# Kernel optimization log

Hardware: AMD Instinct MI355X
Metric: run time of the kernel (lower is better)

The kernel has to match this reference:

```python
import jax, jax.numpy as jnp
import numpy as np

DIM = 128
H = 8
HD = DIM // H
NL = 6
DFF = 2048
EPS = 1e-5
S2S_STEPS = 6


def _ln(x, g, b):
    m = jnp.mean(x, -1, keepdims=True)
    v = jnp.mean(jnp.square(x - m), -1, keepdims=True)
    return (x - m) / jnp.sqrt(v + EPS) * g + b


def _lstm_step(x, h, c, wih, whh, bih, bhh):
    # torch LSTM gate order: i, f, g, o
    gates = x @ wih.T + bih + h @ whh.T + bhh
    i, f, g, o = jnp.split(gates, 4, axis=-1)
    c = jax.nn.sigmoid(f) * c + jax.nn.sigmoid(i) * jnp.tanh(g)
    h = jax.nn.sigmoid(o) * jnp.tanh(c)
    return h, c


def setup_inputs() -> dict:
    key = jax.random.key(0)
    ks = iter(jax.random.split(key, 16))
    n = lambda shape: jax.random.normal(next(ks), shape, jnp.float32) * 0.02
    inp = {
        "data": jax.random.normal(next(ks), (64, 256, 3), jnp.float32),
        "lin0_w": n((DIM, 3)), "lin0_b": jnp.zeros((DIM,), jnp.float32),
        "attn_in_w": n((NL, 3 * DIM, DIM)), "attn_in_b": jnp.zeros((NL, 3 * DIM), jnp.float32),
        "attn_out_w": n((NL, DIM, DIM)), "attn_out_b": jnp.zeros((NL, DIM), jnp.float32),
        "ln1_g": jnp.ones((NL, DIM), jnp.float32), "ln1_b": jnp.zeros((NL, DIM), jnp.float32),
        "ff_w1": n((NL, DFF, DIM)), "ff_b1": jnp.zeros((NL, DFF), jnp.float32),
        "ff_w2": n((NL, DIM, DFF)), "ff_b2": jnp.zeros((NL, DIM), jnp.float32),
        "ln2_g": jnp.ones((NL, DIM), jnp.float32), "ln2_b": jnp.zeros((NL, DIM), jnp.float32),
        "s2s_wih": n((4 * DIM, 2 * DIM)), "s2s_whh": n((4 * DIM, DIM)),
        "s2s_bih": jnp.zeros((4 * DIM,), jnp.float32), "s2s_bhh": jnp.zeros((4 * DIM,), jnp.float32),
        "mem_wih": n((4 * DIM, 2 * DIM)), "mem_whh": n((4 * DIM, DIM)),
        "mem_bih": jnp.zeros((4 * DIM,), jnp.float32), "mem_bhh": jnp.zeros((4 * DIM,), jnp.float32),
        "lin1_w": n((DIM, DIM)), "lin1_b": jnp.zeros((DIM,), jnp.float32),
        "lin3_w": n((1, DIM)), "lin3_b": jnp.zeros((1,), jnp.float32),
    }
    return inp


def reference(data, lin0_w, lin0_b, attn_in_w, attn_in_b, attn_out_w, attn_out_b,
              ln1_g, ln1_b, ff_w1, ff_b1, ff_w2, ff_b2, ln2_g, ln2_b,
              s2s_wih, s2s_whh, s2s_bih, s2s_bhh,
              mem_wih, mem_whh, mem_bih, mem_bhh,
              lin1_w, lin1_b, lin3_w, lin3_b):
    x = jax.nn.relu(data @ lin0_w.T + lin0_b)  # [S=64, B=256, D]
    S, B, _ = x.shape
    # torch TransformerEncoder with batch_first=False: attention over axis 0,
    # axis 1 is the transformer batch. Post-norm layers (norm_first=False), relu FFN.
    for l in range(NL):
        qkv = x @ attn_in_w[l].T + attn_in_b[l]
        q, k, v = jnp.split(qkv, 3, axis=-1)
        q = q.reshape(S, B, H, HD)
        k = k.reshape(S, B, H, HD)
        v = v.reshape(S, B, H, HD)
        scores = jnp.einsum('sbhd,tbhd->bhst', q, k) / np.float32(np.sqrt(HD))
        attn = jax.nn.softmax(scores, axis=-1)
        ao = jnp.einsum('bhst,tbhd->sbhd', attn, v).reshape(S, B, DIM)
        x = _ln(x + ao @ attn_out_w[l].T + attn_out_b[l], ln1_g[l], ln1_b[l])
        ff = jax.nn.relu(x @ ff_w1[l].T + ff_b1[l]) @ ff_w2[l].T + ff_b2[l]
        x = _ln(x + ff, ln2_g[l], ln2_b[l])
    # Set2Set pooling: bidxs assign segment = axis-0 index for each block of
    # num_atoms consecutive rows of flatten(out,0,1), i.e. pool over axis 1.
    q_star = jnp.zeros((S, 2 * DIM), x.dtype)
    h = jnp.zeros((S, DIM), x.dtype)
    c = jnp.zeros((S, DIM), x.dtype)
    for _ in range(S2S_STEPS):
        h, c = _lstm_step(q_star, h, c, s2s_wih, s2s_whh, s2s_bih, s2s_bhh)
        e = jnp.einsum('bnd,bd->bn', x, h)          # [S, num_atoms]
        a = jax.nn.softmax(e, axis=-1)              # segment softmax (uniform segs)
        r = jnp.einsum('bn,bnd->bd', a, x)          # segment weighted sum
        q_star = jnp.concatenate([h, r], axis=-1)   # [S, 2D]
    # memory LSTM: seq_len 1, zero initial state (states=None branch)
    hx = jnp.zeros((S, DIM), x.dtype)
    cx = jnp.zeros((S, DIM), x.dtype)
    hx, cx = _lstm_step(q_star, hx, cx, mem_wih, mem_whh, mem_bih, mem_bhh)
    o = jax.nn.relu(hx @ lin1_w.T + lin1_b)
    v_out = (o @ lin3_w.T + lin3_b)[None]  # [1, S, 1]
    return v_out, hx[None], cx[None]
```

## Files before the change

### kernel.cpp

```cpp
#include <hip/hip_runtime.h>
#include <math.h>


typedef _Float16 __attribute__((ext_vector_type(8))) f16x8;
typedef __attribute__((ext_vector_type(4))) float f32x4;
typedef _Float16 __attribute__((ext_vector_type(2))) h16x2;

__device__ __forceinline__ unsigned short f2h(float f) {
  union { _Float16 h; unsigned short s; } x; x.h = (_Float16)f; return x.s;
}
__device__ __forceinline__ float h2f(unsigned short u) {
  union { unsigned short s; _Float16 h; } x; x.s = u; return (float)x.h;
}
__device__ __forceinline__ unsigned packh(float a, float b) {
  return (unsigned)f2h(a) | ((unsigned)f2h(b) << 16);
}
__device__ __forceinline__ float hlo(unsigned u) {
  union { unsigned short s; _Float16 h; } x; x.s = (unsigned short)(u & 0xffff);
  return (float)x.h;
}
__device__ __forceinline__ float hhi(unsigned u) {
  union { unsigned short s; _Float16 h; } x; x.s = (unsigned short)(u >> 16);
  return (float)x.h;
}
__device__ __forceinline__ float fdot2u(unsigned a, unsigned b, float c) {
#if __has_builtin(__builtin_amdgcn_fdot2)
  union U { unsigned u; h16x2 h; };
  U x, y; x.u = a; y.u = b;
  return __builtin_amdgcn_fdot2(x.h, y.h, c, false);
#else
  return c + hlo(a) * hlo(b) + hhi(a) * hhi(b);
#endif
}
__device__ __forceinline__ float sigf(float x) { return 1.f / (1.f + expf(-x)); }

__device__ __forceinline__ void gl2lds16(const void* g, void* l) {
  __builtin_amdgcn_global_load_lds(
      (const __attribute__((address_space(1))) unsigned int*)g,
      (__attribute__((address_space(3))) unsigned int*)l, 16, 0, 0);
}

__global__ __launch_bounds__(256) void convw_kernel(
    const float* __restrict__ aiw, const float* __restrict__ aow,
    const float* __restrict__ w1, const float* __restrict__ w2,
    const float* __restrict__ wih, const float* __restrict__ whh,
    const float* __restrict__ mwih,
    unsigned short* __restrict__ o0, unsigned short* __restrict__ o1,
    unsigned short* __restrict__ o2, unsigned short* __restrict__ o3,
    unsigned short* __restrict__ o4, unsigned short* __restrict__ o5,
    unsigned short* __restrict__ o6) {
  int i = blockIdx.x * 256 + threadIdx.x;
  if (i < 294912) {
    int l = i / 49152, o = i % 49152;
    int j = o & 7, fr = (o >> 3) & 15, fq = (o >> 7) & 3, ks = (o >> 9) & 3,
        rb = o >> 11;
    o0[i] = f2h(aiw[l * 49152 + (rb * 16 + fr) * 128 + ks * 32 + fq * 8 + j]);
  } else if (i < 393216) {
    int ii = i - 294912;
    int l = ii / 16384, o = ii % 16384;
    int j = o & 7, fr = (o >> 3) & 15, fq = (o >> 7) & 3, ks = (o >> 9) & 3,
        rb = o >> 11;
    o1[ii] = f2h(aow[l * 16384 + (rb * 16 + fr) * 128 + ks * 32 + fq * 8 + j]);
  } else if (i < 1966080) {
    int ii = i - 393216;
    int l = ii >> 18, o = ii & 262143;
    int j = o & 7, fr = (o >> 3) & 15, fq = (o >> 7) & 3, ks = (o >> 9) & 3,
        rb = o >> 11;
    o2[ii] = f2h(w1[l * 262144 + (rb * 16 + fr) * 128 + ks * 32 + fq * 8 + j]);
  } else if (i < 3538944) {
    int ii = i - 1966080;
    int l = ii >> 18, o = ii & 262143;
    int j = o & 7, fr = (o >> 3) & 15, fq = (o >> 7) & 3, ks = (o >> 9) & 63,
        rb = o >> 15;
    o3[ii] = f2h(w2[l * 262144 + (rb * 16 + fr) * 2048 + ks * 32 + fq * 8 + j]);
  } else if (i < 3670016) {
    int j = i - 3538944; o4[j] = f2h(wih[j]);
  } else if (i < 3735552) {
    int j = i - 3670016; o5[j] = f2h(whh[j]);
  } else {
    int j = i - 3735552; o6[j] = f2h(mwih[j]);
  }
}

__global__ __launch_bounds__(256) void lin0_kernel(
    const float* __restrict__ data, const float* __restrict__ w,
    const float* __restrict__ b, float* __restrict__ x,
    unsigned short* __restrict__ xb) {
  int i = blockIdx.x * 256 + threadIdx.x;
  int n = i >> 7, d = i & 127;
  float v = b[d] + data[n * 3 + 0] * w[d * 3 + 0]
                 + data[n * 3 + 1] * w[d * 3 + 1]
                 + data[n * 3 + 2] * w[d * 3 + 2];
  v = fmaxf(v, 0.0f);
  x[i] = v;
  xb[i] = f2h(v);
}

__global__ __launch_bounds__(256, 2) void layer_kernel(
    const unsigned short* __restrict__ xbg,
    const unsigned short* __restrict__ wqkv, const float* __restrict__ bqkv,
    const unsigned short* __restrict__ wout, const float* __restrict__ bout,
    const float* __restrict__ ln1g, const float* __restrict__ ln1b,
    const unsigned short* __restrict__ w1, const float* __restrict__ b1,
    const unsigned short* __restrict__ w2, const float* __restrict__ b2,
    const float* __restrict__ ln2g, const float* __restrict__ ln2b,
    float* __restrict__ xio, unsigned short* __restrict__ xbo) {
  __shared__ __align__(16) unsigned short Xs[64 * 128];
  __shared__ __align__(16) unsigned short QKP[16384];
  __shared__ __align__(16) unsigned short VT[128 * 64];
  __shared__ __align__(16) uint4 zchunk;
  __shared__ float psum[4][32], psq[4][32];
  __shared__ float2 stats[32];

  unsigned short* Qs = QKP;
  unsigned short* Ks2 = QKP + 8192;

  int tid = threadIdx.x, w = tid >> 6, lane = tid & 63;
  int b = blockIdx.x >> 1, half = blockIdx.x & 1;
  int r4 = lane >> 4, cs = lane & 15;
  int fr = lane & 15, fq = lane >> 4;

  if (tid == 0) zchunk = make_uint4(0u, 0u, 0u, 0u);

#pragma unroll
  for (int i = 0; i < 4; i++) {
    int issue = w * 4 + i;
    int row = issue * 4 + r4;
    int g = cs ^ (row & 7);
    gl2lds16(xbg + (size_t)(row * 256 + b) * 128 + g * 8,
             (char*)Xs + issue * 1024);
  }
  __syncthreads();

  f16x8 xfragA[4][4];
#pragma unroll
  for (int ks = 0; ks < 4; ks++)
#pragma unroll
    for (int mi = 0; mi < 4; mi++) {
      int row = mi * 16 + fr;
      int kq = (ks * 4 + fq) ^ (row & 7);
      xfragA[ks][mi] = *(const f16x8*)(Xs + row * 128 + kq * 8);
    }

  {
    f32x4 acc[4][4];
#pragma unroll
    for (int i = 0; i < 4; i++)
#pragma unroll
      for (int j = 0; j < 4; j++) acc[i][j] = (f32x4){0.f, 0.f, 0.f, 0.f};
#pragma unroll
    for (int ks = 0; ks < 4; ks++) {
      f16x8 bf[4];
#pragma unroll
      for (int ni = 0; ni < 4; ni++)
        bf[ni] = *(const f16x8*)(wqkv + (w * 4 + ni) * 2048 + ks * 512 +
                                 fq * 128 + fr * 8);
#pragma unroll
      for (int mi = 0; mi < 4; mi++)
#pragma unroll
        for (int ni = 0; ni < 4; ni++)
          acc[mi][ni] = __builtin_amdgcn_mfma_f32_16x16x32_f16(
              xfragA[ks][mi], bf[ni], acc[mi][ni], 0, 0, 0);
    }
#pragma unroll
    for (int ni = 0; ni < 4; ni++) {
      int c = (w * 4 + ni) * 16 + fr;
      float bv = bqkv[c];
      unsigned short* dst = (c < 128) ? Qs : Ks2;
      int cc = c & 127;
#pragma unroll
      for (int mi = 0; mi < 4; mi++)
#pragma unroll
        for (int r = 0; r < 4; r++) {
          int row = mi * 16 + fq * 4 + r;
          dst[row * 128 + (((cc >> 3) ^ (row & 7)) << 3) + (cc & 7)] =
              f2h(acc[mi][ni][r] + bv);
        }
    }
  }
  __syncthreads();

  {
    f32x4 acc[2][4];
#pragma unroll
    for (int i = 0; i < 2; i++)
#pragma unroll
      for (int j = 0; j < 4; j++) acc[i][j] = (f32x4){0.f, 0.f, 0.f, 0.f};
#pragma unroll
    for (int ks = 0; ks < 4; ks++) {
      f16x8 bf[2];
#pragma unroll
      for (int fi = 0; fi < 2; fi++)
        bf[fi] = *(const f16x8*)(wqkv + (16 + w * 2 + fi) * 2048 + ks * 512 +
                                 fq * 128 + fr * 8);
#pragma unroll
      for (int fi = 0; fi < 2; fi++)
#pragma unroll
        for (int mi = 0; mi < 4; mi++)
          acc[fi][mi] = __builtin_amdgcn_mfma_f32_16x16x32_f16(
              xfragA[ks][mi], bf[fi], acc[fi][mi], 0, 0, 0);
    }
#pragma unroll
    for (int fi = 0; fi < 2; fi++) {
      int f = (w * 2 + fi) * 16 + fr;
      float bv = bqkv[256 + f];
#pragma unroll
      for (int mi = 0; mi < 4; mi++)
#pragma unroll
        for (int r = 0; r < 4; r++) {
          int srow = mi * 16 + fq * 4 + r;
          VT[f * 64 + (((srow >> 3) ^ (f & 7)) << 3) + (srow & 7)] =
              f2h(acc[fi][mi][r] + bv);
        }
    }
  }
  __syncthreads();

  {
    f16x8 afH[2][2], bfH[2][4];
#pragma unroll
    for (int hi = 0; hi < 2; hi++) {
      int h = w * 2 + hi;
#pragma unroll
      for (int mi2 = 0; mi2 < 2; mi2++) {
        int rowg = half * 32 + mi2 * 16 + fr;
        const unsigned short* pa =
            (fq < 2) ? (Qs + rowg * 128 + (((h * 2 + fq) ^ (rowg & 7)) << 3))
                     : (const unsigned short*)&zchunk;
        afH[hi][mi2] = *(const f16x8*)pa;
      }
#pragma unroll
      for (int ti = 0; ti < 4; ti++) {
        int trow = ti * 16 + fr;
        const unsigned short* pb =
            (fq < 2) ? (Ks2 + trow * 128 + (((h * 2 + fq) ^ (trow & 7)) << 3))
                     : (const unsigned short*)&zchunk;
        bfH[hi][ti] = *(const f16x8*)pb;
      }
    }
    __syncthreads();

#pragma unroll
    for (int hi = 0; hi < 2; hi++) {
      int h = w * 2 + hi;
      unsigned short* Pb = QKP + (w * 2 + hi) * 2048;
      f32x4 sc[2][4];
#pragma unroll
      for (int i = 0; i < 2; i++)
#pragma unroll
        for (int j = 0; j < 4; j++) sc[i][j] = (f32x4){0.f, 0.f, 0.f, 0.f};
#pragma unroll
      for (int mi2 = 0; mi2 < 2; mi2++)
#pragma unroll
        for (int ti = 0; ti < 4; ti++)
          sc[mi2][ti] = __builtin_amdgcn_mfma_f32_16x16x32_f16(
              afH[hi][mi2], bfH[hi][ti], sc[mi2][ti], 0, 0, 0);
#pragma unroll
      for (int mi2 = 0; mi2 < 2; mi2++) {
#pragma unroll
        for (int r = 0; r < 4; r++) {
          float m = -1e30f;
#pragma unroll
          for (int ti = 0; ti < 4; ti++) m = fmaxf(m, sc[mi2][ti][r]);
          m = fmaxf(m, __shfl_xor(m, 1, 64));
          m = fmaxf(m, __shfl_xor(m, 2, 64));
          m = fmaxf(m, __shfl_xor(m, 4, 64));
          m = fmaxf(m, __shfl_xor(m, 8, 64));
          m *= 0.25f;
          float ss = 0.f;
#pragma unroll
          for (int ti = 0; ti < 4; ti++) {
            float p = expf(sc[mi2][ti][r] * 0.25f - m);
            sc[mi2][ti][r] = p;
            ss += p;
          }
          ss += __shfl_xor(ss, 1, 64);
          ss += __shfl_xor(ss, 2, 64);
          ss += __shfl_xor(ss, 4, 64);
          ss += __shfl_xor(ss, 8, 64);
          float inv = 1.f / ss;
          int prow = mi2 * 16 + fq * 4 + r;
#pragma unroll
          for (int ti = 0; ti < 4; ti++) {
            int t = ti * 16 + fr;
            Pb[prow * 64 + (((t >> 3) ^ (prow & 7)) << 3) + (t & 7)] =
                f2h(sc[mi2][ti][r] * inv);
          }
        }
      }
      f32x4 po[2];
#pragma unroll
      for (int i = 0; i < 2; i++) po[i] = (f32x4){0.f, 0.f, 0.f, 0.f};
#pragma unroll
      for (int ks2 = 0; ks2 < 2; ks2++) {
        f16x8 af[2], bf;
#pragma unroll
        for (int si2 = 0; si2 < 2; si2++) {
          int prow = si2 * 16 + fr;
          int kq = (ks2 * 4 + fq) ^ (prow & 7);
          af[si2] = *(const f16x8*)(Pb + prow * 64 + kq * 8);
        }
        {
          int vrow = h * 16 + fr;
          int kq = (ks2 * 4 + fq) ^ (vrow & 7);
          bf = *(const f16x8*)(VT + vrow * 64 + kq * 8);
        }
#pragma unroll
        for (int si2 = 0; si2 < 2; si2++)
          po[si2] = __builtin_amdgcn_mfma_f32_16x16x32_f16(af[si2], bf,
                                                           po[si2], 0, 0, 0);
      }
#pragma unroll
      for (int si2 = 0; si2 < 2; si2++)
#pragma unroll
        for (int r = 0; r < 4; r++) {
          int arow = si2 * 16 + fq * 4 + r;
          int c = h * 16 + fr;
          Xs[arow * 128 + (((c >> 3) ^ (arow & 7)) << 3) + (c & 7)] =
              f2h(po[si2][r]);
        }
    }
  }
  __syncthreads();

  float vv4[2][2][4];
  {
    f32x4 acc[2][2];
#pragma unroll
    for (int i = 0; i < 2; i++)
#pragma unroll
      for (int j = 0; j < 2; j++) acc[i][j] = (f32x4){0.f, 0.f, 0.f, 0.f};
#pragma unroll
    for (int ks = 0; ks < 4; ks++) {
      f16x8 af[2], bwo[2];
#pragma unroll
      for (int si2 = 0; si2 < 2; si2++) {
        int rowl = si2 * 16 + fr;
        int kq = (ks * 4 + fq) ^ (rowl & 7);
        af[si2] = *(const f16x8*)(Xs + rowl * 128 + kq * 8);
      }
#pragma unroll
      for (int ni = 0; ni < 2; ni++)
        bwo[ni] = *(const f16x8*)(wout + (w * 2 + ni) * 2048 + ks * 512 +
                                  fq * 128 + fr * 8);
#pragma unroll
      for (int si2 = 0; si2 < 2; si2++)
#pragma unroll
        for (int ni = 0; ni < 2; ni++)
          acc[si2][ni] = __builtin_amdgcn_mfma_f32_16x16x32_f16(
              af[si2], bwo[ni], acc[si2][ni], 0, 0, 0);
    }
    float sums[2][4], sqs[2][4];
#pragma unroll
    for (int si2 = 0; si2 < 2; si2++)
#pragma unroll
      for (int r = 0; r < 4; r++) { sums[si2][r] = 0.f; sqs[si2][r] = 0.f; }
#pragma unroll
    for (int ni = 0; ni < 2; ni++) {
      int c = (w * 2 + ni) * 16 + fr;
      float bv = bout[c];
#pragma unroll
      for (int si2 = 0; si2 < 2; si2++)
#pragma unroll
        for (int r = 0; r < 4; r++) {
          int rowl = si2 * 16 + fq * 4 + r;
          int rowg = half * 32 + rowl;
          float v = acc[si2][ni][r] + bv + xio[(size_t)(rowg * 256 + b) * 128 + c];
          vv4[ni][si2][r] = v;
          sums[si2][r] += v;
          sqs[si2][r] += v * v;
        }
    }
#pragma unroll
    for (int d = 1; d < 16; d <<= 1) {
#pragma unroll
      for (int si2 = 0; si2 < 2; si2++)
#pragma unroll
        for (int r = 0; r < 4; r++) {
          sums[si2][r] += __shfl_xor(sums[si2][r], d, 64);
          sqs[si2][r] += __shfl_xor(sqs[si2][r], d, 64);
        }
    }
    if (fr == 0) {
#pragma unroll
      for (int si2 = 0; si2 < 2; si2++)
#pragma unroll
        for (int r = 0; r < 4; r++) {
          int rowl = si2 * 16 + fq * 4 + r;
          psum[w][rowl] = sums[si2][r];
          psq[w][rowl] = sqs[si2][r];
        }
    }
    __syncthreads();
    if (tid < 32) {
      float S = 0.f, Q = 0.f;
#pragma unroll
      for (int ww = 0; ww < 4; ww++) { S += psum[ww][tid]; Q += psq[ww][tid]; }
      float m = S * (1.f / 128.f);
      float var = Q * (1.f / 128.f) - m * m;
      stats[tid] = make_float2(m, rsqrtf(var + 1e-5f));
    }
    __syncthreads();
#pragma unroll
    for (int ni = 0; ni < 2; ni++) {
      int c = (w * 2 + ni) * 16 + fr;
      float gl = ln1g[c], bl = ln1b[c];
#pragma unroll
      for (int si2 = 0; si2 < 2; si2++)
#pragma unroll
        for (int r = 0; r < 4; r++) {
          int rowl = si2 * 16 + fq * 4 + r;
          float2 st2 = stats[rowl];
          float y = (vv4[ni][si2][r] - st2.x) * st2.y * gl + bl;
          Xs[rowl * 128 + (((c >> 3) ^ (rowl & 7)) << 3) + (c & 7)] = f2h(y);
        }
    }
  }
  __syncthreads();

  f16x8 xfragF[4][2];
#pragma unroll
  for (int ks = 0; ks < 4; ks++)
#pragma unroll
    for (int mi2 = 0; mi2 < 2; mi2++) {
      int rowl = mi2 * 16 + fr;
      int kq = (ks * 4 + fq) ^ (rowl & 7);
      xfragF[ks][mi2] = *(const f16x8*)(Xs + rowl * 128 + kq * 8);
    }

  f32x4 acc2[2][2];
#pragma unroll
  for (int i = 0; i < 2; i++)
#pragma unroll
    for (int j = 0; j < 2; j++) acc2[i][j] = (f32x4){0.f, 0.f, 0.f, 0.f};

  for (int c = 0; c < 16; c++) {
    unsigned short* Hcur = QKP + (c & 1) * 4096;
    f32x4 acc1[2][2];
#pragma unroll
    for (int i = 0; i < 2; i++)
#pragma unroll
      for (int j = 0; j < 2; j++) acc1[i][j] = (f32x4){0.f, 0.f, 0.f, 0.f};
#pragma unroll
    for (int ks = 0; ks < 4; ks++) {
      f16x8 b1f[2];
#pragma unroll
      for (int ni = 0; ni < 2; ni++)
        b1f[ni] = *(const f16x8*)(w1 + (size_t)(c * 8 + w * 2 + ni) * 2048 +
                                  ks * 512 + fq * 128 + fr * 8);
#pragma unroll
      for (int mi2 = 0; mi2 < 2; mi2++)
#pragma unroll
        for (int ni = 0; ni < 2; ni++)
          acc1[mi2][ni] = __builtin_amdgcn_mfma_f32_16x16x32_f16(
              xfragF[ks][mi2], b1f[ni], acc1[mi2][ni], 0, 0, 0);
    }
#pragma unroll
    for (int ni = 0; ni < 2; ni++) {
      int col = (w * 2 + ni) * 16 + fr;
      float bv = b1[c * 128 + col];
#pragma unroll
      for (int mi2 = 0; mi2 < 2; mi2++)
#pragma unroll
        for (int r = 0; r < 4; r++) {
          int rowl = mi2 * 16 + fq * 4 + r;
          Hcur[rowl * 128 + (((col >> 3) ^ (rowl & 7)) << 3) + (col & 7)] =
              f2h(fmaxf(acc1[mi2][ni][r] + bv, 0.f));
        }
    }
    __syncthreads();
#pragma unroll
    for (int ks = 0; ks < 4; ks++) {
      f16x8 af[2], b2f[2];
#pragma unroll
      for (int si2 = 0; si2 < 2; si2++) {
        int rowl = si2 * 16 + fr;
        int kq = (ks * 4 + fq) ^ (rowl & 7);
        af[si2] = *(const f16x8*)(Hcur + rowl * 128 + kq * 8);
      }
#pragma unroll
      for (int ni = 0; ni < 2; ni++)
        b2f[ni] = *(const f16x8*)(w2 + (size_t)(w * 2 + ni) * 32768 +
                                  (c * 4 + ks) * 512 + fq * 128 + fr * 8);
#pragma unroll
      for (int si2 = 0; si2 < 2; si2++)
#pragma unroll
        for (int ni = 0; ni < 2; ni++)
          acc2[si2][ni] = __builtin_amdgcn_mfma_f32_16x16x32_f16(
              af[si2], b2f[ni], acc2[si2][ni], 0, 0, 0);
    }
  }

  {
    float vvo[2][2][4];
    float sums[2][4], sqs[2][4];
#pragma unroll
    for (int si2 = 0; si2 < 2; si2++)
#pragma unroll
      for (int r = 0; r < 4; r++) { sums[si2][r] = 0.f; sqs[si2][r] = 0.f; }
#pragma unroll
    for (int ni = 0; ni < 2; ni++) {
      int c = (w * 2 + ni) * 16 + fr;
      float bv = b2[c];
#pragma unroll
      for (int si2 = 0; si2 < 2; si2++)
#pragma unroll
        for (int r = 0; r < 4; r++) {
          int rowl = si2 * 16 + fq * 4 + r;
          float resid =
              h2f(Xs[rowl * 128 + (((c >> 3) ^ (rowl & 7)) << 3) + (c & 7)]);
          float v = acc2[si2][ni][r] + bv + resid;
          vvo[ni][si2][r] = v;
          sums[si2][r] += v;
          sqs[si2][r] += v * v;
        }
    }
#pragma unroll
    for (int d = 1; d < 16; d <<= 1) {
#pragma unroll
      for (int si2 = 0; si2 < 2; si2++)
#pragma unroll
        for (int r = 0; r < 4; r++) {
          sums[si2][r] += __shfl_xor(sums[si2][r], d, 64);
          sqs[si2][r] += __shfl_xor(sqs[si2][r], d, 64);
        }
    }
    if (fr == 0) {
#pragma unroll
      for (int si2 = 0; si2 < 2; si2++)
#pragma unroll
        for (int r = 0; r < 4; r++) {
          int rowl = si2 * 16 + fq * 4 + r;
          psum[w][rowl] = sums[si2][r];
          psq[w][rowl] = sqs[si2][r];
        }
    }
    __syncthreads();
    if (tid < 32) {
      float S = 0.f, Q = 0.f;
#pragma unroll
      for (int ww = 0; ww < 4; ww++) { S += psum[ww][tid]; Q += psq[ww][tid]; }
      float m = S * (1.f / 128.f);
      float var = Q * (1.f / 128.f) - m * m;
      stats[tid] = make_float2(m, rsqrtf(var + 1e-5f));
    }
    __syncthreads();
#pragma unroll
    for (int ni = 0; ni < 2; ni++) {
      int c = (w * 2 + ni) * 16 + fr;
      float gl = ln2g[c], bl = ln2b[c];
#pragma unroll
      for (int si2 = 0; si2 < 2; si2++)
#pragma unroll
        for (int r = 0; r < 4; r++) {
          int rowl = si2 * 16 + fq * 4 + r;
          float2 st = stats[rowl];
          float y = (vvo[ni][si2][r] - st.x) * st.y * gl + bl;
          size_t o = (size_t)((half * 32 + rowl) * 256 + b) * 128 + c;
          xio[o] = y;
          xbo[o] = f2h(y);
        }
    }
  }
}

__global__ __launch_bounds__(512, 1) void s2s_kernel(
    const unsigned short* __restrict__ xb,
    const unsigned short* __restrict__ wihh,
    const unsigned short* __restrict__ whhh,
    const float* __restrict__ bih, const float* __restrict__ bhh,
    const unsigned short* __restrict__ mwihh,
    const float* __restrict__ mbih, const float* __restrict__ mbhh,
    const float* __restrict__ l1w, const float* __restrict__ l1b,
    const float* __restrict__ l3w, const float* __restrict__ l3b,
    float* __restrict__ out) {
  __shared__ __align__(16) unsigned xl[256 * 65];
  __shared__ __align__(16) unsigned qu[128];
  __shared__ __align__(16) float cst[128];
  __shared__ __align__(16) float gates[512];
  __shared__ __align__(16) float red[256];
  __shared__ __align__(16) float aw[256];
  int s = blockIdx.x, t = threadIdx.x, lane = t & 63, w = t >> 6;

  uint4 wreg[32], ureg[16];
  {
    const uint4* wp = (const uint4*)(wihh + (size_t)t * 256);
#pragma unroll
    for (int i = 0; i < 32; i++) wreg[i] = wp[i];
    const uint4* up = (const uint4*)(whhh + (size_t)t * 128);
#pragma unroll
    for (int i = 0; i < 16; i++) ureg[i] = up[i];
  }

  const uint4* xs4 = (const uint4*)(xb + (size_t)s * 32768);
#pragma unroll
  for (int it = 0; it < 8; it++) {
    int f = it * 512 + t;
    uint4 v = xs4[f];
    int n = f >> 4, jc = (f & 15) * 4;
    unsigned* dst = xl + n * 65 + jc;
    dst[0] = v.x; dst[1] = v.y; dst[2] = v.z; dst[3] = v.w;
  }
  if (t < 128) cst[t] = 0.f;
  __syncthreads();

  const uint4* q4 = (const uint4*)qu;
  float bsum = bih[t] + bhh[t];

  for (int step = 0; step < 6; step++) {
    if (step > 0) {
      float a0 = 0.f, a1 = 0.f, a2 = 0.f, a3 = 0.f;
#pragma unroll
      for (int i = 0; i < 16; i++) {
        uint4 qv = q4[i];
        a0 = fdot2u(wreg[i].x, qv.x, a0);
        a1 = fdot2u(wreg[i].y, qv.y, a1);
        a2 = fdot2u(wreg[i].z, qv.z, a2);
        a3 = fdot2u(wreg[i].w, qv.w, a3);
        a0 = fdot2u(ureg[i].x, qv.x, a0);
        a1 = fdot2u(ureg[i].y, qv.y, a1);
        a2 = fdot2u(ureg[i].z, qv.z, a2);
        a3 = fdot2u(ureg[i].w, qv.w, a3);
      }
#pragma unroll
      for (int i = 16; i < 32; i++) {
        uint4 qv = q4[i];
        a0 = fdot2u(wreg[i].x, qv.x, a0);
        a1 = fdot2u(wreg[i].y, qv.y, a1);
        a2 = fdot2u(wreg[i].z, qv.z, a2);
        a3 = fdot2u(wreg[i].w, qv.w, a3);
      }
      gates[t] = bsum + ((a0 + a1) + (a2 + a3));
    } else {
      gates[t] = bsum;
    }
    __syncthreads();
    if (t < 128) {
      float ig = sigf(gates[t]), fg = sigf(gates[128 + t]);
      float gg = tanhf(gates[256 + t]), og = sigf(gates[384 + t]);
      float cn = fg * cst[t] + ig * gg;
      cst[t] = cn;
      float hn = og * tanhf(cn);
      float hp = __shfl_xor(hn, 1, 64);
      if ((t & 1) == 0) qu[t >> 1] = packh(hn, hp);
    }
    __syncthreads();
    if (step > 0) {
      int n = t >> 1, p = t & 1;
      const unsigned* xr = xl + n * 65 + p * 32;
      float e0 = 0.f, e1 = 0.f;
#pragma unroll 8
      for (int i = 0; i < 32; i += 2) {
        e0 = fdot2u(xr[i], qu[p * 32 + i], e0);
        e1 = fdot2u(xr[i + 1], qu[p * 32 + i + 1], e1);
      }
      float e = e0 + e1;
      e += __shfl_xor(e, 1, 64);
      if (p == 0) red[n] = e;
      __syncthreads();
      float v0 = red[lane], v1 = red[64 + lane];
      float v2 = red[128 + lane], v3 = red[192 + lane];
      float m = fmaxf(fmaxf(v0, v1), fmaxf(v2, v3));
#pragma unroll
      for (int d = 1; d < 64; d <<= 1) m = fmaxf(m, __shfl_xor(m, d, 64));
      float p0 = expf(v0 - m), p1 = expf(v1 - m);
      float p2 = expf(v2 - m), p3 = expf(v3 - m);
      float ss = p0 + p1 + p2 + p3;
#pragma unroll
      for (int d = 1; d < 64; d <<= 1) ss += __shfl_xor(ss, d, 64);
      float Sinv = 1.f / ss;
      if (w == 0) {
        aw[lane] = p0 * Sinv; aw[64 + lane] = p1 * Sinv;
        aw[128 + lane] = p2 * Sinv; aw[192 + lane] = p3 * Sinv;
      }
    } else {
      if (t < 256) aw[t] = 1.f / 256.f;
    }
    __syncthreads();
    {
      int d = t & 127, grp = t >> 7;
      const unsigned* xc = xl + grp * 64 * 65 + (d >> 1);
      int hi = d & 1;
      const float* ap = aw + grp * 64;
      float r = 0.f;
#pragma unroll 8
      for (int n2 = 0; n2 < 64; n2++) {
        unsigned u = xc[n2 * 65];
        r += ap[n2] * (hi ? hhi(u) : hlo(u));
      }
      gates[t] = r;
    }
    __syncthreads();
    if (t < 128) {
      float rd = gates[t] + gates[128 + t] + gates[256 + t] + gates[384 + t];
      float rp = __shfl_xor(rd, 1, 64);
      if ((t & 1) == 0) qu[64 + (t >> 1)] = packh(rd, rp);
    }
    __syncthreads();
  }
  {
    float a0 = 0.f, a1 = 0.f, a2 = 0.f, a3 = 0.f;
    const uint4* mp = (const uint4*)(mwihh + (size_t)t * 256);
#pragma unroll 8
    for (int i = 0; i < 32; i++) {
      uint4 wv = mp[i], qv = q4[i];
      a0 = fdot2u(wv.x, qv.x, a0);
      a1 = fdot2u(wv.y, qv.y, a1);
      a2 = fdot2u(wv.z, qv.z, a2);
      a3 = fdot2u(wv.w, qv.w, a3);
    }
    gates[t] = mbih[t] + mbhh[t] + ((a0 + a1) + (a2 + a3));
  }
  __syncthreads();
  if (t < 128) {
    float ig = sigf(gates[t]);
    float gg = tanhf(gates[256 + t]);
    float og = sigf(gates[384 + t]);
    float cx = ig * gg;
    float hx = og * tanhf(cx);
    cst[t] = hx;
    out[64 + s * 128 + t] = hx;
    out[64 + 8192 + s * 128 + t] = cx;
  }
  __syncthreads();
  if (t < 128) {
    float acc = l1b[t];
    const float4* w4 = (const float4*)(l1w + (size_t)t * 128);
    const float4* h4 = (const float4*)cst;
#pragma unroll 8
    for (int k = 0; k < 32; k++) {
      float4 a = w4[k], b = h4[k];
      acc += a.x * b.x + a.y * b.y + a.z * b.z + a.w * b.w;
    }
    red[t] = fmaxf(acc, 0.f) * l3w[t];
  } else if (t < 256) {
    red[t] = 0.f;
  }
  __syncthreads();
  for (int off = 128; off; off >>= 1) {
    if (t < off) red[t] += red[t + off];
    __syncthreads();
  }
  if (t == 0) out[s] = red[0] + l3b[0];
}

extern "C" void kernel_launch(void* const* d_in, const int* in_sizes, int n_in,
                              void* d_out, int out_size, void* d_ws,
                              size_t ws_size, hipStream_t stream) {
  const float* data       = (const float*)d_in[0];
  const float* lin0_w     = (const float*)d_in[1];
  const float* lin0_b     = (const float*)d_in[2];
  const float* attn_in_w  = (const float*)d_in[3];
  const float* attn_in_b  = (const float*)d_in[4];
  const float* attn_out_w = (const float*)d_in[5];
  const float* attn_out_b = (const float*)d_in[6];
  const float* ln1_g      = (const float*)d_in[7];
  const float* ln1_b      = (const float*)d_in[8];
  const float* ff_w1      = (const float*)d_in[9];
  const float* ff_b1      = (const float*)d_in[10];
  const float* ff_w2      = (const float*)d_in[11];
  const float* ff_b2      = (const float*)d_in[12];
  const float* ln2_g      = (const float*)d_in[13];
  const float* ln2_b      = (const float*)d_in[14];
  const float* s2s_wih    = (const float*)d_in[15];
  const float* s2s_whh    = (const float*)d_in[16];
  const float* s2s_bih    = (const float*)d_in[17];
  const float* s2s_bhh    = (const float*)d_in[18];
  const float* mem_wih    = (const float*)d_in[19];
  const float* mem_bih    = (const float*)d_in[21];
  const float* mem_bhh    = (const float*)d_in[22];
  const float* lin1_w     = (const float*)d_in[23];
  const float* lin1_b     = (const float*)d_in[24];
  const float* lin3_w     = (const float*)d_in[25];
  const float* lin3_b     = (const float*)d_in[26];
  float* out = (float*)d_out;

  char* p = (char*)d_ws;
  float* x = (float*)p;                      p += (size_t)16384 * 128 * 4;
  unsigned short* xb = (unsigned short*)p;   p += (size_t)16384 * 128 * 2;
  unsigned short* wqkv = (unsigned short*)p; p += (size_t)294912 * 2;
  unsigned short* wout = (unsigned short*)p; p += (size_t)98304 * 2;
  unsigned short* w1h = (unsigned short*)p;  p += (size_t)1572864 * 2;
  unsigned short* w2h = (unsigned short*)p;  p += (size_t)1572864 * 2;
  unsigned short* wihh = (unsigned short*)p; p += (size_t)131072 * 2;
  unsigned short* whhh = (unsigned short*)p; p += (size_t)65536 * 2;
  unsigned short* mwihh = (unsigned short*)p; p += (size_t)131072 * 2;

  convw_kernel<<<15104, 256, 0, stream>>>(
      attn_in_w, attn_out_w, ff_w1, ff_w2, s2s_wih, s2s_whh, mem_wih,
      wqkv, wout, w1h, w2h, wihh, whhh, mwihh);
  lin0_kernel<<<8192, 256, 0, stream>>>(data, lin0_w, lin0_b, x, xb);

  for (int l = 0; l < 6; l++) {
    layer_kernel<<<512, 256, 0, stream>>>(
        xb, wqkv + (size_t)l * 49152, attn_in_b + l * 384,
        wout + (size_t)l * 16384, attn_out_b + l * 128,
        ln1_g + l * 128, ln1_b + l * 128,
        w1h + (size_t)l * 262144, ff_b1 + l * 2048,
        w2h + (size_t)l * 262144, ff_b2 + l * 128,
        ln2_g + l * 128, ln2_b + l * 128, x, xb);
  }

  s2s_kernel<<<64, 512, 0, stream>>>(
      xb, wihh, whhh, s2s_bih, s2s_bhh,
      mwihh, mem_bih, mem_bhh, lin1_w, lin1_b, lin3_w, lin3_b, out);
}
```

Baseline: 461.5 us.

## Use 8 waves per layer block and overlay shared memory buffers

The transformer layer kernel now runs 512 threads (8 waves) per block instead of 256. Each wave handles one attention head and one 16-column slice of every projection and FFN chunk, and the QKV projection is merged into a single pass with 3 column tiles per wave. Shared memory is reorganised into one overlaid buffer, with Q stored only for this block's half of the rows, which cuts LDS use so more blocks can stay resident. The aim is higher occupancy and more latency hiding, at the cost of extra barriers, a smaller per-wave MFMA tile, and every wave recomputing all 64 rows of K and V.

```diff
diff --git a/kernel.cpp b/kernel.cpp
--- a/kernel.cpp
+++ b/kernel.cpp
@@ -96,7 +96,7 @@
   xb[i] = f2h(v);
 }
 
-__global__ __launch_bounds__(256, 2) void layer_kernel(
+__global__ __launch_bounds__(512, 4) void layer_kernel(
     const unsigned short* __restrict__ xbg,
     const unsigned short* __restrict__ wqkv, const float* __restrict__ bqkv,
     const unsigned short* __restrict__ wout, const float* __restrict__ bout,
@@ -105,26 +105,28 @@
     const unsigned short* __restrict__ w2, const float* __restrict__ b2,
     const float* __restrict__ ln2g, const float* __restrict__ ln2b,
     float* __restrict__ xio, unsigned short* __restrict__ xbo) {
-  __shared__ __align__(16) unsigned short Xs[64 * 128];
-  __shared__ __align__(16) unsigned short QKP[16384];
-  __shared__ __align__(16) unsigned short VT[128 * 64];
-  __shared__ __align__(16) uint4 zchunk;
-  __shared__ float psum[4][32], psq[4][32];
-  __shared__ float2 stats[32];
-
-  unsigned short* Qs = QKP;
-  unsigned short* Ks2 = QKP + 8192;
+  __shared__ __align__(16) unsigned short SM[25736];
+  unsigned short* Xs = SM;
+  unsigned short* Qs = SM + 4096;
+  unsigned short* Ks = SM + 8192;
+  unsigned short* VT = SM + 16384;
+  unsigned short* AOs = SM + 16384;
+  unsigned short* Xn = SM;
+  float* psum = (float*)(SM + 24576);
+  float* psq = (float*)(SM + 25088);
+  float2* stats = (float2*)(SM + 25600);
+  uint4* zch = (uint4*)(SM + 25728);
 
   int tid = threadIdx.x, w = tid >> 6, lane = tid & 63;
   int b = blockIdx.x >> 1, half = blockIdx.x & 1;
   int r4 = lane >> 4, cs = lane & 15;
   int fr = lane & 15, fq = lane >> 4;
 
-  if (tid == 0) zchunk = make_uint4(0u, 0u, 0u, 0u);
-
-#pragma unroll
-  for (int i = 0; i < 4; i++) {
-    int issue = w * 4 + i;
+  if (tid == 0) *zch = make_uint4(0u, 0u, 0u, 0u);
+
+#pragma unroll
+  for (int i = 0; i < 2; i++) {
+    int issue = w * 2 + i;
     int row = issue * 4 + r4;
     int g = cs ^ (row & 7);
     gl2lds16(xbg + (size_t)(row * 256 + b) * 128 + g * 8,
@@ -141,236 +143,206 @@
       int kq = (ks * 4 + fq) ^ (row & 7);
       xfragA[ks][mi] = *(const f16x8*)(Xs + row * 128 + kq * 8);
     }
+  __syncthreads();
 
   {
-    f32x4 acc[4][4];
+    f32x4 acc[4][3];
 #pragma unroll
     for (int i = 0; i < 4; i++)
 #pragma unroll
-      for (int j = 0; j < 4; j++) acc[i][j] = (f32x4){0.f, 0.f, 0.f, 0.f};
+      for (int j = 0; j < 3; j++) acc[i][j] = (f32x4){0.f, 0.f, 0.f, 0.f};
 #pragma unroll
     for (int ks = 0; ks < 4; ks++) {
-      f16x8 bf[4];
-#pragma unroll
-      for (int ni = 0; ni < 4; ni++)
-        bf[ni] = *(const f16x8*)(wqkv + (w * 4 + ni) * 2048 + ks * 512 +
-                                 fq * 128 + fr * 8);
+      f16x8 bf[3];
+#pragma unroll
+      for (int ni = 0; ni < 3; ni++)
+        bf[ni] = *(const f16x8*)(wqkv + (size_t)(w * 3 + ni) * 2048 +
+                                 ks * 512 + fq * 128 + fr * 8);
 #pragma unroll
       for (int mi = 0; mi < 4; mi++)
 #pragma unroll
-        for (int ni = 0; ni < 4; ni++)
+        for (int ni = 0; ni < 3; ni++)
           acc[mi][ni] = __builtin_amdgcn_mfma_f32_16x16x32_f16(
               xfragA[ks][mi], bf[ni], acc[mi][ni], 0, 0, 0);
     }
 #pragma unroll
-    for (int ni = 0; ni < 4; ni++) {
-      int c = (w * 4 + ni) * 16 + fr;
+    for (int ni = 0; ni < 3; ni++) {
+      int c = (w * 3 + ni) * 16 + fr;
       float bv = bqkv[c];
-      unsigned short* dst = (c < 128) ? Qs : Ks2;
-      int cc = c & 127;
-#pragma unroll
-      for (int mi = 0; mi < 4; mi++)
-#pragma unroll
-        for (int r = 0; r < 4; r++) {
-          int row = mi * 16 + fq * 4 + r;
-          dst[row * 128 + (((cc >> 3) ^ (row & 7)) << 3) + (cc & 7)] =
-              f2h(acc[mi][ni][r] + bv);
-        }
-    }
-  }
-  __syncthreads();
-
-  {
-    f32x4 acc[2][4];
-#pragma unroll
-    for (int i = 0; i < 2; i++)
-#pragma unroll
-      for (int j = 0; j < 4; j++) acc[i][j] = (f32x4){0.f, 0.f, 0.f, 0.f};
-#pragma unroll
-    for (int ks = 0; ks < 4; ks++) {
-      f16x8 bf[2];
-#pragma unroll
-      for (int fi = 0; fi < 2; fi++)
-        bf[fi] = *(const f16x8*)(wqkv + (16 + w * 2 + fi) * 2048 + ks * 512 +
-                                 fq * 128 + fr * 8);
-#pragma unroll
-      for (int fi = 0; fi < 2; fi++)
-#pragma unroll
-        for (int mi = 0; mi < 4; mi++)
-          acc[fi][mi] = __builtin_amdgcn_mfma_f32_16x16x32_f16(
-              xfragA[ks][mi], bf[fi], acc[fi][mi], 0, 0, 0);
-    }
-#pragma unroll
-    for (int fi = 0; fi < 2; fi++) {
-      int f = (w * 2 + fi) * 16 + fr;
-      float bv = bqkv[256 + f];
-#pragma unroll
-      for (int mi = 0; mi < 4; mi++)
-#pragma unroll
-        for (int r = 0; r < 4; r++) {
-          int srow = mi * 16 + fq * 4 + r;
-          VT[f * 64 + (((srow >> 3) ^ (f & 7)) << 3) + (srow & 7)] =
-              f2h(acc[fi][mi][r] + bv);
-        }
-    }
-  }
-  __syncthreads();
-
-  {
-    f16x8 afH[2][2], bfH[2][4];
-#pragma unroll
-    for (int hi = 0; hi < 2; hi++) {
-      int h = w * 2 + hi;
-#pragma unroll
-      for (int mi2 = 0; mi2 < 2; mi2++) {
-        int rowg = half * 32 + mi2 * 16 + fr;
-        const unsigned short* pa =
-            (fq < 2) ? (Qs + rowg * 128 + (((h * 2 + fq) ^ (rowg & 7)) << 3))
-                     : (const unsigned short*)&zchunk;
-        afH[hi][mi2] = *(const f16x8*)pa;
-      }
-#pragma unroll
-      for (int ti = 0; ti < 4; ti++) {
-        int trow = ti * 16 + fr;
-        const unsigned short* pb =
-            (fq < 2) ? (Ks2 + trow * 128 + (((h * 2 + fq) ^ (trow & 7)) << 3))
-                     : (const unsigned short*)&zchunk;
-        bfH[hi][ti] = *(const f16x8*)pb;
-      }
-    }
-    __syncthreads();
-
-#pragma unroll
-    for (int hi = 0; hi < 2; hi++) {
-      int h = w * 2 + hi;
-      unsigned short* Pb = QKP + (w * 2 + hi) * 2048;
-      f32x4 sc[2][4];
-#pragma unroll
-      for (int i = 0; i < 2; i++)
-#pragma unroll
-        for (int j = 0; j < 4; j++) sc[i][j] = (f32x4){0.f, 0.f, 0.f, 0.f};
-#pragma unroll
-      for (int mi2 = 0; mi2 < 2; mi2++)
-#pragma unroll
-        for (int ti = 0; ti < 4; ti++)
-          sc[mi2][ti] = __builtin_amdgcn_mfma_f32_16x16x32_f16(
-              afH[hi][mi2], bfH[hi][ti], sc[mi2][ti], 0, 0, 0);
-#pragma unroll
-      for (int mi2 = 0; mi2 < 2; mi2++) {
-#pragma unroll
-        for (int r = 0; r < 4; r++) {
-          float m = -1e30f;
-#pragma unroll
-          for (int ti = 0; ti < 4; ti++) m = fmaxf(m, sc[mi2][ti][r]);
-          m = fmaxf(m, __shfl_xor(m, 1, 64));
-          m = fmaxf(m, __shfl_xor(m, 2, 64));
-          m = fmaxf(m, __shfl_xor(m, 4, 64));
-          m = fmaxf(m, __shfl_xor(m, 8, 64));
-          m *= 0.25f;
-          float ss = 0.f;
-#pragma unroll
-          for (int ti = 0; ti < 4; ti++) {
-            float p = expf(sc[mi2][ti][r] * 0.25f - m);
-            sc[mi2][ti][r] = p;
-            ss += p;
-          }
-          ss += __shfl_xor(ss, 1, 64);
-          ss += __shfl_xor(ss, 2, 64);
-          ss += __shfl_xor(ss, 4, 64);
-          ss += __shfl_xor(ss, 8, 64);
-          float inv = 1.f / ss;
-          int prow = mi2 * 16 + fq * 4 + r;
-#pragma unroll
-          for (int ti = 0; ti < 4; ti++) {
-            int t = ti * 16 + fr;
-            Pb[prow * 64 + (((t >> 3) ^ (prow & 7)) << 3) + (t & 7)] =
-                f2h(sc[mi2][ti][r] * inv);
+      if (c < 128) {
+#pragma unroll
+        for (int mi2 = 0; mi2 < 2; mi2++) {
+          int mi = half * 2 + mi2;
+#pragma unroll
+          for (int r = 0; r < 4; r++) {
+            int prow = mi2 * 16 + fq * 4 + r;
+            Qs[prow * 128 + (((c >> 3) ^ (prow & 7)) << 3) + (c & 7)] =
+                f2h(acc[mi][ni][r] + bv);
           }
         }
-      }
-      f32x4 po[2];
-#pragma unroll
-      for (int i = 0; i < 2; i++) po[i] = (f32x4){0.f, 0.f, 0.f, 0.f};
-#pragma unroll
-      for (int ks2 = 0; ks2 < 2; ks2++) {
-        f16x8 af[2], bf;
-#pragma unroll
-        for (int si2 = 0; si2 < 2; si2++) {
-          int prow = si2 * 16 + fr;
-          int kq = (ks2 * 4 + fq) ^ (prow & 7);
-          af[si2] = *(const f16x8*)(Pb + prow * 64 + kq * 8);
+      } else if (c < 256) {
+        int cc = c - 128;
+#pragma unroll
+        for (int mi = 0; mi < 4; mi++)
+#pragma unroll
+          for (int r = 0; r < 4; r++) {
+            int row = mi * 16 + fq * 4 + r;
+            Ks[row * 128 + (((cc >> 3) ^ (row & 7)) << 3) + (cc & 7)] =
+                f2h(acc[mi][ni][r] + bv);
+          }
+      } else {
+        int f = c - 256;
+#pragma unroll
+        for (int mi = 0; mi < 4; mi++)
+#pragma unroll
+          for (int r = 0; r < 4; r++) {
+            int srow = mi * 16 + fq * 4 + r;
+            VT[f * 64 + (((srow >> 3) ^ (f & 7)) << 3) + (srow & 7)] =
+                f2h(acc[mi][ni][r] + bv);
+          }
+      }
+    }
+  }
+  __syncthreads();
+
+  f32x4 po[2];
+  {
+    int h = w;
+    f16x8 afH[2], bfH[4];
+#pragma unroll
+    for (int mi2 = 0; mi2 < 2; mi2++) {
+      int qrow = mi2 * 16 + fr;
+      const unsigned short* pa =
+          (fq < 2) ? (Qs + qrow * 128 + (((h * 2 + fq) ^ (qrow & 7)) << 3))
+                   : (const unsigned short*)zch;
+      afH[mi2] = *(const f16x8*)pa;
+    }
+#pragma unroll
+    for (int ti = 0; ti < 4; ti++) {
+      int trow = ti * 16 + fr;
+      const unsigned short* pb =
+          (fq < 2) ? (Ks + trow * 128 + (((h * 2 + fq) ^ (trow & 7)) << 3))
+                   : (const unsigned short*)zch;
+      bfH[ti] = *(const f16x8*)pb;
+    }
+    __syncthreads();
+
+    unsigned short* Pb = SM + w * 2048;
+    f32x4 sc[2][4];
+#pragma unroll
+    for (int i = 0; i < 2; i++)
+#pragma unroll
+      for (int j = 0; j < 4; j++) sc[i][j] = (f32x4){0.f, 0.f, 0.f, 0.f};
+#pragma unroll
+    for (int mi2 = 0; mi2 < 2; mi2++)
+#pragma unroll
+      for (int ti = 0; ti < 4; ti++)
+        sc[mi2][ti] = __builtin_amdgcn_mfma_f32_16x16x32_f16(
+            afH[mi2], bfH[ti], sc[mi2][ti], 0, 0, 0);
+#pragma unroll
+    for (int mi2 = 0; mi2 < 2; mi2++) {
+#pragma unroll
+      for (int r = 0; r < 4; r++) {
+        float m = -1e30f;
+#pragma unroll
+        for (int ti = 0; ti < 4; ti++) m = fmaxf(m, sc[mi2][ti][r]);
+        m = fmaxf(m, __shfl_xor(m, 1, 64));
+        m = fmaxf(m, __shfl_xor(m, 2, 64));
+        m = fmaxf(m, __shfl_xor(m, 4, 64));
+        m = fmaxf(m, __shfl_xor(m, 8, 64));
+        m *= 0.25f;
+        float ss = 0.f;
+#pragma unroll
+        for (int ti = 0; ti < 4; ti++) {
+          float p = expf(sc[mi2][ti][r] * 0.25f - m);
+          sc[mi2][ti][r] = p;
+          ss += p;
         }
-        {
-          int vrow = h * 16 + fr;
-          int kq = (ks2 * 4 + fq) ^ (vrow & 7);
-          bf = *(const f16x8*)(VT + vrow * 64 + kq * 8);
+        ss += __shfl_xor(ss, 1, 64);
+        ss += __shfl_xor(ss, 2, 64);
+        ss += __shfl_xor(ss, 4, 64);
+        ss += __shfl_xor(ss, 8, 64);
+        float inv = 1.f / ss;
+        int prow = mi2 * 16 + fq * 4 + r;
+#pragma unroll
+        for (int ti = 0; ti < 4; ti++) {
+          int t = ti * 16 + fr;
+          Pb[prow * 64 + (((t >> 3) ^ (prow & 7)) << 3) + (t & 7)] =
+              f2h(sc[mi2][ti][r] * inv);
         }
-#pragma unroll
-        for (int si2 = 0; si2 < 2; si2++)
-          po[si2] = __builtin_amdgcn_mfma_f32_16x16x32_f16(af[si2], bf,
-                                                           po[si2], 0, 0, 0);
+      }
+    }
+#pragma unroll
+    for (int i = 0; i < 2; i++) po[i] = (f32x4){0.f, 0.f, 0.f, 0.f};
+#pragma unroll
+    for (int ks2 = 0; ks2 < 2; ks2++) {
+      f16x8 af[2], bf;
+#pragma unroll
+      for (int si2 = 0; si2 < 2; si2++) {
+        int prow = si2 * 16 + fr;
+        int kq = (ks2 * 4 + fq) ^ (prow & 7);
+        af[si2] = *(const f16x8*)(Pb + prow * 64 + kq * 8);
+      }
+      {
+        int vrow = h * 16 + fr;
+        int kq = (ks2 * 4 + fq) ^ (vrow & 7);
+        bf = *(const f16x8*)(VT + vrow * 64 + kq * 8);
       }
 #pragma unroll
       for (int si2 = 0; si2 < 2; si2++)
-#pragma unroll
-        for (int r = 0; r < 4; r++) {
-          int arow = si2 * 16 + fq * 4 + r;
-          int c = h * 16 + fr;
-          Xs[arow * 128 + (((c >> 3) ^ (arow & 7)) << 3) + (c & 7)] =
-              f2h(po[si2][r]);
-        }
-    }
-  }
-  __syncthreads();
-
-  float vv4[2][2][4];
+        po[si2] = __builtin_amdgcn_mfma_f32_16x16x32_f16(af[si2], bf, po[si2],
+                                                         0, 0, 0);
+    }
+  }
+  __syncthreads();
   {
-    f32x4 acc[2][2];
-#pragma unroll
-    for (int i = 0; i < 2; i++)
-#pragma unroll
-      for (int j = 0; j < 2; j++) acc[i][j] = (f32x4){0.f, 0.f, 0.f, 0.f};
+    int h = w;
+#pragma unroll
+    for (int si2 = 0; si2 < 2; si2++)
+#pragma unroll
+      for (int r = 0; r < 4; r++) {
+        int arow = si2 * 16 + fq * 4 + r;
+        int c = h * 16 + fr;
+        AOs[arow * 128 + (((c >> 3) ^ (arow & 7)) << 3) + (c & 7)] =
+            f2h(po[si2][r]);
+      }
+  }
+  __syncthreads();
+
+  {
+    f32x4 acc[2];
+#pragma unroll
+    for (int i = 0; i < 2; i++) acc[i] = (f32x4){0.f, 0.f, 0.f, 0.f};
 #pragma unroll
     for (int ks = 0; ks < 4; ks++) {
-      f16x8 af[2], bwo[2];
+      f16x8 af[2];
 #pragma unroll
       for (int si2 = 0; si2 < 2; si2++) {
         int rowl = si2 * 16 + fr;
         int kq = (ks * 4 + fq) ^ (rowl & 7);
-        af[si2] = *(const f16x8*)(Xs + rowl * 128 + kq * 8);
-      }
-#pragma unroll
-      for (int ni = 0; ni < 2; ni++)
-        bwo[ni] = *(const f16x8*)(wout + (w * 2 + ni) * 2048 + ks * 512 +
+        af[si2] = *(const f16x8*)(AOs + rowl * 128 + kq * 8);
+      }
+      f16x8 bwo = *(const f16x8*)(wout + (size_t)w * 2048 + ks * 512 +
                                   fq * 128 + fr * 8);
 #pragma unroll
       for (int si2 = 0; si2 < 2; si2++)
-#pragma unroll
-        for (int ni = 0; ni < 2; ni++)
-          acc[si2][ni] = __builtin_amdgcn_mfma_f32_16x16x32_f16(
-              af[si2], bwo[ni], acc[si2][ni], 0, 0, 0);
-    }
-    float sums[2][4], sqs[2][4];
+        acc[si2] = __builtin_amdgcn_mfma_f32_16x16x32_f16(af[si2], bwo,
+                                                          acc[si2], 0, 0, 0);
+    }
+    int c = w * 16 + fr;
+    float bv = bout[c];
+    float vv4[2][4], sums[2][4], sqs[2][4];
 #pragma unroll
     for (int si2 = 0; si2 < 2; si2++)
 #pragma unroll
-      for (int r = 0; r < 4; r++) { sums[si2][r] = 0.f; sqs[si2][r] = 0.f; }
-#pragma unroll
-    for (int ni = 0; ni < 2; ni++) {
-      int c = (w * 2 + ni) * 16 + fr;
-      float bv = bout[c];
-#pragma unroll
-      for (int si2 = 0; si2 < 2; si2++)
-#pragma unroll
-        for (int r = 0; r < 4; r++) {
-          int rowl = si2 * 16 + fq * 4 + r;
-          int rowg = half * 32 + rowl;
-          float v = acc[si2][ni][r] + bv + xio[(size_t)(rowg * 256 + b) * 128 + c];
-          vv4[ni][si2][r] = v;
-          sums[si2][r] += v;
-          sqs[si2][r] += v * v;
-        }
-    }
+      for (int r = 0; r < 4; r++) {
+        int rowl = si2 * 16 + fq * 4 + r;
+        int rowg = half * 32 + rowl;
+        float v = acc[si2][r] + bv + xio[(size_t)(rowg * 256 + b) * 128 + c];
+        vv4[si2][r] = v;
+        sums[si2][r] = v;
+        sqs[si2][r] = v * v;
+      }
 #pragma unroll
     for (int d = 1; d < 16; d <<= 1) {
 #pragma unroll
@@ -387,34 +359,33 @@
 #pragma unroll
         for (int r = 0; r < 4; r++) {
           int rowl = si2 * 16 + fq * 4 + r;
-          psum[w][rowl] = sums[si2][r];
-          psq[w][rowl] = sqs[si2][r];
+          psum[w * 32 + rowl] = sums[si2][r];
+          psq[w * 32 + rowl] = sqs[si2][r];
         }
     }
     __syncthreads();
     if (tid < 32) {
       float S = 0.f, Q = 0.f;
 #pragma unroll
-      for (int ww = 0; ww < 4; ww++) { S += psum[ww][tid]; Q += psq[ww][tid]; }
+      for (int ww = 0; ww < 8; ww++) {
+        S += psum[ww * 32 + tid];
+        Q += psq[ww * 32 + tid];
+      }
       float m = S * (1.f / 128.f);
       float var = Q * (1.f / 128.f) - m * m;
       stats[tid] = make_float2(m, rsqrtf(var + 1e-5f));
     }
     __syncthreads();
-#pragma unroll
-    for (int ni = 0; ni < 2; ni++) {
-      int c = (w * 2 + ni) * 16 + fr;
-      float gl = ln1g[c], bl = ln1b[c];
-#pragma unroll
-      for (int si2 = 0; si2 < 2; si2++)
-#pragma unroll
-        for (int r = 0; r < 4; r++) {
-          int rowl = si2 * 16 + fq * 4 + r;
-          float2 st2 = stats[rowl];
-          float y = (vv4[ni][si2][r] - st2.x) * st2.y * gl + bl;
-          Xs[rowl * 128 + (((c >> 3) ^ (rowl & 7)) << 3) + (c & 7)] = f2h(y);
-        }
-    }
+    float gl = ln1g[c], bl = ln1b[c];
+#pragma unroll
+    for (int si2 = 0; si2 < 2; si2++)
+#pragma unroll
+      for (int r = 0; r < 4; r++) {
+        int rowl = si2 * 16 + fq * 4 + r;
+        float2 st2 = stats[rowl];
+        float y = (vv4[si2][r] - st2.x) * st2.y * gl + bl;
+        Xn[rowl * 128 + (((c >> 3) ^ (rowl & 7)) << 3) + (c & 7)] = f2h(y);
+      }
   }
   __syncthreads();
 
@@ -425,39 +396,31 @@
     for (int mi2 = 0; mi2 < 2; mi2++) {
       int rowl = mi2 * 16 + fr;
       int kq = (ks * 4 + fq) ^ (rowl & 7);
-      xfragF[ks][mi2] = *(const f16x8*)(Xs + rowl * 128 + kq * 8);
-    }
-
-  f32x4 acc2[2][2];
-#pragma unroll
-  for (int i = 0; i < 2; i++)
-#pragma unroll
-    for (int j = 0; j < 2; j++) acc2[i][j] = (f32x4){0.f, 0.f, 0.f, 0.f};
+      xfragF[ks][mi2] = *(const f16x8*)(Xn + rowl * 128 + kq * 8);
+    }
+
+  unsigned short* HsB = SM + 8192;
+  f32x4 acc2[2];
+#pragma unroll
+  for (int i = 0; i < 2; i++) acc2[i] = (f32x4){0.f, 0.f, 0.f, 0.f};
 
   for (int c = 0; c < 16; c++) {
-    unsigned short* Hcur = QKP + (c & 1) * 4096;
-    f32x4 acc1[2][2];
-#pragma unroll
-    for (int i = 0; i < 2; i++)
-#pragma unroll
-      for (int j = 0; j < 2; j++) acc1[i][j] = (f32x4){0.f, 0.f, 0.f, 0.f};
+    unsigned short* Hcur = HsB + (c & 1) * 4096;
+    f32x4 acc1[2];
+#pragma unroll
+    for (int i = 0; i < 2; i++) acc1[i] = (f32x4){0.f, 0.f, 0.f, 0.f};
 #pragma unroll
     for (int ks = 0; ks < 4; ks++) {
-      f16x8 b1f[2];
-#pragma unroll
-      for (int ni = 0; ni < 2; ni++)
-        b1f[ni] = *(const f16x8*)(w1 + (size_t)(c * 8 + w * 2 + ni) * 2048 +
-                                  ks * 512 + fq * 128 + fr * 8);
+      f16x8 b1f = *(const f16x8*)(w1 + (size_t)(c * 8 + w) * 2048 + ks * 512 +
+                                  fq * 128 + fr * 8);
 #pragma unroll
       for (int mi2 = 0; mi2 < 2; mi2++)
-#pragma unroll
-        for (int ni = 0; ni < 2; ni++)
-          acc1[mi2][ni] = __builtin_amdgcn_mfma_f32_16x16x32_f16(
-              xfragF[ks][mi2], b1f[ni], acc1[mi2][ni], 0, 0, 0);
-    }
-#pragma unroll
-    for (int ni = 0; ni < 2; ni++) {
-      int col = (w * 2 + ni) * 16 + fr;
+        acc1[mi2] = __builtin_amdgcn_mfma_f32_16x16x32_f16(xfragF[ks][mi2],
+                                                           b1f, acc1[mi2],
+                                                           0, 0, 0);
+    }
+    {
+      int col = w * 16 + fr;
       float bv = b1[c * 128 + col];
 #pragma unroll
       for (int mi2 = 0; mi2 < 2; mi2++)
@@ -465,56 +428,44 @@
         for (int r = 0; r < 4; r++) {
           int rowl = mi2 * 16 + fq * 4 + r;
           Hcur[rowl * 128 + (((col >> 3) ^ (rowl & 7)) << 3) + (col & 7)] =
-              f2h(fmaxf(acc1[mi2][ni][r] + bv, 0.f));
+              f2h(fmaxf(acc1[mi2][r] + bv, 0.f));
         }
     }
     __syncthreads();
 #pragma unroll
     for (int ks = 0; ks < 4; ks++) {
-      f16x8 af[2], b2f[2];
+      f16x8 af[2];
 #pragma unroll
       for (int si2 = 0; si2 < 2; si2++) {
         int rowl = si2 * 16 + fr;
         int kq = (ks * 4 + fq) ^ (rowl & 7);
         af[si2] = *(const f16x8*)(Hcur + rowl * 128 + kq * 8);
       }
-#pragma unroll
-      for (int ni = 0; ni < 2; ni++)
-        b2f[ni] = *(const f16x8*)(w2 + (size_t)(w * 2 + ni) * 32768 +
-                                  (c * 4 + ks) * 512 + fq * 128 + fr * 8);
+      f16x8 b2f = *(const f16x8*)(w2 + (size_t)w * 32768 + (c * 4 + ks) * 512 +
+                                  fq * 128 + fr * 8);
 #pragma unroll
       for (int si2 = 0; si2 < 2; si2++)
-#pragma unroll
-        for (int ni = 0; ni < 2; ni++)
-          acc2[si2][ni] = __builtin_amdgcn_mfma_f32_16x16x32_f16(
-              af[si2], b2f[ni], acc2[si2][ni], 0, 0, 0);
+        acc2[si2] = __builtin_amdgcn_mfma_f32_16x16x32_f16(af[si2], b2f,
+                                                           acc2[si2], 0, 0, 0);
     }
   }
 
   {
-    float vvo[2][2][4];
-    float sums[2][4], sqs[2][4];
+    int c = w * 16 + fr;
+    float bv = b2[c];
+    float vvo[2][4], sums[2][4], sqs[2][4];
 #pragma unroll
     for (int si2 = 0; si2 < 2; si2++)
 #pragma unroll
-      for (int r = 0; r < 4; r++) { sums[si2][r] = 0.f; sqs[si2][r] = 0.f; }
-#pragma unroll
-    for (int ni = 0; ni < 2; ni++) {
-      int c = (w * 2 + ni) * 16 + fr;
-      float bv = b2[c];
-#pragma unroll
-      for (int si2 = 0; si2 < 2; si2++)
-#pragma unroll
-        for (int r = 0; r < 4; r++) {
-          int rowl = si2 * 16 + fq * 4 + r;
-          float resid =
-              h2f(Xs[rowl * 128 + (((c >> 3) ^ (rowl & 7)) << 3) + (c & 7)]);
-          float v = acc2[si2][ni][r] + bv + resid;
-          vvo[ni][si2][r] = v;
-          sums[si2][r] += v;
-          sqs[si2][r] += v * v;
-        }
-    }
+      for (int r = 0; r < 4; r++) {
+        int rowl = si2 * 16 + fq * 4 + r;
+        float resid =
+            h2f(Xn[rowl * 128 + (((c >> 3) ^ (rowl & 7)) << 3) + (c & 7)]);
+        float v = acc2[si2][r] + bv + resid;
+        vvo[si2][r] = v;
+        sums[si2][r] = v;
+        sqs[si2][r] = v * v;
+      }
 #pragma unroll
     for (int d = 1; d < 16; d <<= 1) {
 #pragma unroll
@@ -531,36 +482,35 @@
 #pragma unroll
         for (int r = 0; r < 4; r++) {
           int rowl = si2 * 16 + fq * 4 + r;
-          psum[w][rowl] = sums[si2][r];
-          psq[w][rowl] = sqs[si2][r];
+          psum[w * 32 + rowl] = sums[si2][r];
+          psq[w * 32 + rowl] = sqs[si2][r];
         }
     }
     __syncthreads();
     if (tid < 32) {
       float S = 0.f, Q = 0.f;
 #pragma unroll
-      for (int ww = 0; ww < 4; ww++) { S += psum[ww][tid]; Q += psq[ww][tid]; }
+      for (int ww = 0; ww < 8; ww++) {
+        S += psum[ww * 32 + tid];
+        Q += psq[ww * 32 + tid];
+      }
       float m = S * (1.f / 128.f);
       float var = Q * (1.f / 128.f) - m * m;
       stats[tid] = make_float2(m, rsqrtf(var + 1e-5f));
     }
     __syncthreads();
-#pragma unroll
-    for (int ni = 0; ni < 2; ni++) {
-      int c = (w * 2 + ni) * 16 + fr;
-      float gl = ln2g[c], bl = ln2b[c];
-#pragma unroll
-      for (int si2 = 0; si2 < 2; si2++)
-#pragma unroll
-        for (int r = 0; r < 4; r++) {
-          int rowl = si2 * 16 + fq * 4 + r;
-          float2 st = stats[rowl];
-          float y = (vvo[ni][si2][r] - st.x) * st.y * gl + bl;
-          size_t o = (size_t)((half * 32 + rowl) * 256 + b) * 128 + c;
-          xio[o] = y;
-          xbo[o] = f2h(y);
-        }
-    }
+    float gl = ln2g[c], bl = ln2b[c];
+#pragma unroll
+    for (int si2 = 0; si2 < 2; si2++)
+#pragma unroll
+      for (int r = 0; r < 4; r++) {
+        int rowl = si2 * 16 + fq * 4 + r;
+        float2 st = stats[rowl];
+        float y = (vvo[si2][r] - st.x) * st.y * gl + bl;
+        size_t o = (size_t)((half * 32 + rowl) * 256 + b) * 128 + c;
+        xio[o] = y;
+        xbo[o] = f2h(y);
+      }
   }
 }
 
@@ -792,7 +742,7 @@
   lin0_kernel<<<8192, 256, 0, stream>>>(data, lin0_w, lin0_b, x, xb);
 
   for (int l = 0; l < 6; l++) {
-    layer_kernel<<<512, 256, 0, stream>>>(
+    layer_kernel<<<512, 512, 0, stream>>>(
         xb, wqkv + (size_t)l * 49152, attn_in_b + l * 384,
         wout + (size_t)l * 16384, attn_out_b + l * 128,
         ln1_g + l * 128, ln1_b + l * 128,
```

Result: no change. 463.5 us (+0.4%).
